# Kernel tuning notes

Hardware: AMD Instinct MI355X
Metric: run time of the kernel (lower is better)

## Reference

```python
import jax, jax.numpy as jnp
import numpy as np

N = 25000
E = 400000
H = 4        # heads
C = 256      # per-head channels
D_IN = 1024
NEG_SLOPE = 0.2


def setup_inputs() -> dict:
    key = jax.random.key(0)
    k1, k2, k3, k4, k5, k6 = jax.random.split(key, 6)
    x = jax.random.normal(k1, (N, D_IN), dtype=jnp.float32)
    edge_index = jax.random.randint(k2, (2, E), 0, N, dtype=jnp.int64)
    # GATConv parameters
    scale = 1.0 / np.sqrt(D_IN)
    W = jax.random.normal(k3, (D_IN, H * C), dtype=jnp.float32) * scale
    att_src = jax.random.normal(k4, (H, C), dtype=jnp.float32) * 0.1
    att_dst = jax.random.normal(k5, (H, C), dtype=jnp.float32) * 0.1
    bias = jax.random.normal(k6, (H * C,), dtype=jnp.float32) * 0.01
    return {"x": x, "edge_index": edge_index, "W": W,
            "att_src": att_src, "att_dst": att_dst, "bias": bias}


def reference(x, edge_index, W, att_src, att_dst, bias):
    # Dense projection: [N, D_IN] @ [D_IN, H*C] -> [N, H, C]
    xp = (x @ W).reshape(N, H, C)

    # Per-node attention logits [N, H]
    a_src = jnp.einsum('nhc,hc->nh', xp, att_src)
    a_dst = jnp.einsum('nhc,hc->nh', xp, att_dst)

    # PyG default add_self_loops=True
    loops = jnp.arange(N, dtype=edge_index.dtype)
    src = jnp.concatenate([edge_index[0], loops])  # [E+N]
    dst = jnp.concatenate([edge_index[1], loops])  # [E+N]

    # Edge attention logits + LeakyReLU
    e = jax.nn.leaky_relu(a_src[src] + a_dst[dst], NEG_SLOPE)  # [E+N, H]

    # Segment softmax over destination nodes (every node has a self loop)
    m = jax.ops.segment_max(e, dst, num_segments=N)            # [N, H]
    ee = jnp.exp(e - m[dst])
    z = jax.ops.segment_sum(ee, dst, num_segments=N)           # [N, H]
    alpha = ee / z[dst]                                        # [E+N, H]

    # Scatter-weighted aggregation: out[i] = sum_j alpha_ij * xp[j]
    msgs = xp[src] * alpha[:, :, None]                         # [E+N, H, C]
    out = jax.ops.segment_sum(msgs, dst, num_segments=N)       # [N, H, C]

    out = out.reshape(N, H * C) + bias
    # dropout(0.5) is identity in eval mode; act = ReLU
    return jax.nn.relu(out)
```

## Files before the change

### kernel.cpp

```cpp
#include <hip/hip_runtime.h>
#include <hip/hip_bf16.h>
#include <stdint.h>

#define N_NODES 25000
#define M_PAD   25088
#define E_EDGES 400000
#define NE      (E_EDGES + N_NODES)
#define D_DIM   1024
#define NEG_SLOPE 0.2f
#define KMAX    64

using bf16x8  = __attribute__((ext_vector_type(8))) short;
using floatx4 = __attribute__((ext_vector_type(4))) float;
using ushort8 = __attribute__((ext_vector_type(8))) unsigned short;

__device__ __forceinline__ unsigned short f2bf(float f) {
    union { float f; unsigned u; } v{f};
    unsigned r = v.u + 0x7fffu + ((v.u >> 16) & 1u);
    return (unsigned short)(r >> 16);
}
__device__ __forceinline__ float bf2f(unsigned short s) {
    union { unsigned u; float f; } v{(unsigned)s << 16};
    return v.f;
}

__global__ __launch_bounds__(256) void k_prep(
        const float* __restrict__ x, const float* __restrict__ W,
        unsigned short* __restrict__ xb, unsigned short* __restrict__ Wt,
        int* __restrict__ cursor) {
    __shared__ float tile[32][33];
    const int b = blockIdx.x, t = threadIdx.x;
    if (b < 1024) {
        int bx = b & 31, by = b >> 5;
        int tx = t & 31, ty = t >> 5;
        #pragma unroll
        for (int i = 0; i < 32; i += 8)
            tile[ty + i][tx] = W[(size_t)(by * 32 + ty + i) * D_DIM + bx * 32 + tx];
        __syncthreads();
        #pragma unroll
        for (int i = 0; i < 32; i += 8)
            Wt[(size_t)(bx * 32 + ty + i) * D_DIM + by * 32 + tx] =
                f2bf(tile[tx][ty + i]);
        if (b < 98) {
            int idx = b * 256 + t;
            if (idx < N_NODES) cursor[idx] = 0;
        }
    } else {
        int i = (b - 1024) * 256 + t;
        int row = i >> 8;
        ushort4 o;
        if (row < N_NODES) {
            float4 v = ((const float4*)x)[i];
            o = make_ushort4(f2bf(v.x), f2bf(v.y), f2bf(v.z), f2bf(v.w));
        } else {
            o = make_ushort4(0, 0, 0, 0);
        }
        ((ushort4*)xb)[i] = o;
    }
}

__device__ __forceinline__ void stage_half16(
        const unsigned short* __restrict__ g,
        unsigned short* lds_half,
        int wave, int rl, int sl8) {
    #pragma unroll
    for (int j = 0; j < 2; ++j) {
        const int R = j * 64 + wave * 8;
        __builtin_amdgcn_global_load_lds(
            (const __attribute__((address_space(1))) void*)
                (g + (size_t)(R + rl) * 1024 + sl8),
            (__attribute__((address_space(3))) void*)(lds_half + R * 64),
            16, 0, 0);
    }
}

__global__ __launch_bounds__(512, 2) void k_gemm256(
        const unsigned short* __restrict__ A,
        const unsigned short* __restrict__ Bt,
        const float* __restrict__ att_src, const float* __restrict__ att_dst,
        unsigned short* __restrict__ C,
        float* __restrict__ a_src, float* __restrict__ a_dst) {
    __shared__ unsigned short lds[65536];

    const int tid  = threadIdx.x;
    const int wave = tid >> 6, lane = tid & 63;
    const int lrow = lane & 15, quad = lane >> 4;
    const int wm   = wave >> 2, wn = wave & 3;
    const int rl   = lane >> 3;
    const int sl8  = ((lane & 7) ^ rl) * 8;

    const int wg = (blockIdx.x & 7) * 49 + (blockIdx.x >> 3);
    const int m0 = (wg % 98) * 256;
    const int n0 = (wg / 98) * 256;

    const unsigned short* Am = A  + (size_t)m0 * 1024;
    const unsigned short* Bn = Bt + (size_t)n0 * 1024;

    const int colk0 = (quad * 8)      ^ ((lrow & 7) << 3);
    const int colk1 = (32 + quad * 8) ^ ((lrow & 7) << 3);

    floatx4 acc[8][4] = {};

    stage_half16(Bn,                          lds + 16384,               wave, rl, sl8);
    stage_half16(Bn + (size_t)128 * 1024,     lds + 16384 + 8192,        wave, rl, sl8);
    stage_half16(Am,                          lds,                       wave, rl, sl8);
    stage_half16(Am + (size_t)128 * 1024,     lds + 8192,                wave, rl, sl8);
    stage_half16(Bn + 64,                     lds + 49152,               wave, rl, sl8);
    stage_half16(Bn + (size_t)128 * 1024 + 64, lds + 49152 + 8192,       wave, rl, sl8);
    stage_half16(Am + 64,                     lds + 32768,               wave, rl, sl8);
    asm volatile("s_waitcnt vmcnt(6)" ::: "memory");
    __builtin_amdgcn_sched_barrier(0);
    __builtin_amdgcn_s_barrier();

    #pragma unroll 1
    for (int it = 0; it < 8; ++it) {
        const int t   = it * 2;
        const int kt1 = t * 64 + 64, kt2 = t * 64 + 128, kt3 = t * 64 + 192;
        const bool s1 = kt2 < 1024;
        const bool s2 = kt3 < 1024;
        #pragma unroll
        for (int hb = 0; hb < 2; ++hb) {
            const unsigned short* LAc = lds + hb * 32768;
            const unsigned short* LBc = LAc + 16384;
            bf16x8 bfr[4][2];
            #pragma unroll
            for (int q = 0; q < 4; ++q) {
                bf16x8 af[2][2];
                #pragma unroll
                for (int j = 0; j < 2; ++j) {
                    const int ar = (wm * 128 + (2 * q + j) * 16 + lrow) * 64;
                    af[j][0] = *(const bf16x8*)(LAc + ar + colk0);
                    af[j][1] = *(const bf16x8*)(LAc + ar + colk1);
                }
                if (q == 0) {
                    #pragma unroll
                    for (int ni = 0; ni < 4; ++ni) {
                        const int br = (wn * 64 + ni * 16 + lrow) * 64;
                        bfr[ni][0] = *(const bf16x8*)(LBc + br + colk0);
                        bfr[ni][1] = *(const bf16x8*)(LBc + br + colk1);
                    }
                }
                if (hb == 0) {
                    if (q == 0)
                        stage_half16(Am + (size_t)128 * 1024 + kt1,
                                     lds + 32768 + 8192, wave, rl, sl8);
                    if (q == 1 && s1)
                        stage_half16(Bn + kt2, lds + 16384, wave, rl, sl8);
                    if (q == 2 && s1)
                        stage_half16(Bn + (size_t)128 * 1024 + kt2,
                                     lds + 16384 + 8192, wave, rl, sl8);
                    if (q == 3 && s1)
                        stage_half16(Am + kt2, lds, wave, rl, sl8);
                } else {
                    if (q == 0 && s1)
                        stage_half16(Am + (size_t)128 * 1024 + kt2,
                                     lds + 8192, wave, rl, sl8);
                    if (q == 1 && s2)
                        stage_half16(Bn + kt3, lds + 49152, wave, rl, sl8);
                    if (q == 2 && s2)
                        stage_half16(Bn + (size_t)128 * 1024 + kt3,
                                     lds + 49152 + 8192, wave, rl, sl8);
                    if (q == 3 && s2)
                        stage_half16(Am + kt3, lds + 32768, wave, rl, sl8);
                }
                if (q == 3) {
                    const bool full = (hb == 0) ? s1 : s2;
                    if (full) asm volatile("s_waitcnt vmcnt(6)" ::: "memory");
                    else      asm volatile("s_waitcnt vmcnt(0)" ::: "memory");
                    __builtin_amdgcn_sched_barrier(0);
                }
                __builtin_amdgcn_s_barrier();
                asm volatile("s_waitcnt lgkmcnt(0)" ::: "memory");
                __builtin_amdgcn_sched_barrier(0);
                __builtin_amdgcn_s_setprio(1);
                #pragma unroll
                for (int j = 0; j < 2; ++j)
                    #pragma unroll
                    for (int ni = 0; ni < 4; ++ni) {
                        acc[2*q+j][ni] = __builtin_amdgcn_mfma_f32_16x16x32_bf16(
                            af[j][0], bfr[ni][0], acc[2*q+j][ni], 0, 0, 0);
                        acc[2*q+j][ni] = __builtin_amdgcn_mfma_f32_16x16x32_bf16(
                            af[j][1], bfr[ni][1], acc[2*q+j][ni], 0, 0, 0);
                    }
                __builtin_amdgcn_s_setprio(0);
                __builtin_amdgcn_s_barrier();
            }
        }
    }

    {
        const int h4 = n0 >> 8;
        float asv[4], adv[4];
        #pragma unroll
        for (int ni = 0; ni < 4; ++ni) {
            int gc = n0 + wn * 64 + ni * 16 + lrow;
            asv[ni] = att_src[gc];
            adv[ni] = att_dst[gc];
        }
        __syncthreads();
        float* red = (float*)lds;
        #pragma unroll
        for (int mi = 0; mi < 8; ++mi) {
            #pragma unroll
            for (int r = 0; r < 4; ++r) {
                float s = 0.f, d = 0.f;
                #pragma unroll
                for (int ni = 0; ni < 4; ++ni) {
                    s += acc[mi][ni][r] * asv[ni];
                    d += acc[mi][ni][r] * adv[ni];
                }
                #pragma unroll
                for (int off = 1; off < 16; off <<= 1) {
                    s += __shfl_xor(s, off);
                    d += __shfl_xor(d, off);
                }
                if (lrow == 0) {
                    int rowl = mi * 16 + quad * 4 + r;
                    red[((wn * 2 + wm) * 128 + rowl) * 2 + 0] = s;
                    red[((wn * 2 + wm) * 128 + rowl) * 2 + 1] = d;
                }
            }
        }
        __syncthreads();
        const int sd   = tid & 1;
        const int rowl = (tid >> 1) & 127;
        const int wmr  = tid >> 8;
        float v = red[((0 * 2 + wmr) * 128 + rowl) * 2 + sd]
                + red[((1 * 2 + wmr) * 128 + rowl) * 2 + sd]
                + red[((2 * 2 + wmr) * 128 + rowl) * 2 + sd]
                + red[((3 * 2 + wmr) * 128 + rowl) * 2 + sd];
        int gm = m0 + wmr * 128 + rowl;
        if (gm < N_NODES) {
            if (sd == 0) a_src[gm * 4 + h4] = v;
            else         a_dst[gm * 4 + h4] = v;
        }
    }

    #pragma unroll
    for (int mi = 0; mi < 8; ++mi)
        #pragma unroll
        for (int ni = 0; ni < 4; ++ni)
            #pragma unroll
            for (int r = 0; r < 4; ++r) {
                int gm = m0 + wm * 128 + mi * 16 + quad * 4 + r;
                int gn = n0 + wn * 64 + ni * 16 + lrow;
                C[(size_t)gm * 1024 + gn] = f2bf(acc[mi][ni][r]);
            }
}

__global__ __launch_bounds__(256) void k_edge_exp_scatter(
        const int* __restrict__ ei,
        const float* __restrict__ a_src, const float* __restrict__ a_dst,
        int* __restrict__ cursor,
        int* __restrict__ csr_src, float* __restrict__ csr_ee) {
    int e = blockIdx.x * 256 + threadIdx.x;
    if (e >= NE) return;
    int s, d;
    if (e < E_EDGES) { s = ei[e]; d = ei[E_EDGES + e]; }
    else             { s = d = e - E_EDGES; }
    float4 as = *(const float4*)(&a_src[s * 4]);
    float4 ad = *(const float4*)(&a_dst[d * 4]);
    float l0 = as.x + ad.x, l1 = as.y + ad.y, l2 = as.z + ad.z, l3 = as.w + ad.w;
    l0 = l0 > 0.f ? l0 : NEG_SLOPE * l0;
    l1 = l1 > 0.f ? l1 : NEG_SLOPE * l1;
    l2 = l2 > 0.f ? l2 : NEG_SLOPE * l2;
    l3 = l3 > 0.f ? l3 : NEG_SLOPE * l3;
    int pos = atomicAdd(&cursor[d], 1);
    if (pos < KMAX) {
        int slot = d * KMAX + pos;
        csr_src[slot] = s;
        *(float4*)(&csr_ee[(size_t)slot * 4]) =
            make_float4(__expf(l0), __expf(l1), __expf(l2), __expf(l3));
    }
}

__device__ __forceinline__ void acc8(float* acc, float a, ushort8 v) {
    #pragma unroll
    for (int j = 0; j < 8; ++j) acc[j] += a * bf2f((unsigned short)v[j]);
}

__global__ __launch_bounds__(256) void k_node_aggregate(
        const int* __restrict__ csr_src, const float* __restrict__ csr_ee,
        const int* __restrict__ degc,
        const unsigned short* __restrict__ xp,
        const float* __restrict__ bias, float* __restrict__ out) {
    const int tid   = threadIdx.x;
    const int wave  = tid >> 6;
    const int lane  = tid & 63;
    const int n     = blockIdx.x * 2 + (wave >> 1);
    const int chalf = wave & 1;
    const int row   = n * KMAX;
    int deg = degc[n];
    deg = deg < KMAX ? deg : KMAX;

    float z0 = 0.f, z1 = 0.f, z2 = 0.f, z3 = 0.f;
    if (lane < deg) {
        float4 v = *(const float4*)(&csr_ee[(size_t)(row + lane) * 4]);
        z0 = v.x; z1 = v.y; z2 = v.z; z3 = v.w;
    }
    #pragma unroll
    for (int off = 32; off > 0; off >>= 1) {
        z0 += __shfl_down(z0, off);
        z1 += __shfl_down(z1, off);
        z2 += __shfl_down(z2, off);
        z3 += __shfl_down(z3, off);
    }
    z0 = __shfl(z0, 0); z1 = __shfl(z1, 0);
    z2 = __shfl(z2, 0); z3 = __shfl(z3, 0);

    const int c = chalf * 512 + lane * 8;
    const int h = c >> 8;
    const float rz = 1.0f / (chalf ? (lane >= 32 ? z3 : z2)
                                   : (lane >= 32 ? z1 : z0));

    float acc[8] = {};
    int i = 0;
    for (; i + 8 <= deg; i += 8) {
        int s[8];
        float a[8];
        #pragma unroll
        for (int u = 0; u < 8; ++u) s[u] = csr_src[row + i + u];
        #pragma unroll
        for (int u = 0; u < 8; ++u) a[u] = csr_ee[(size_t)(row + i + u) * 4 + h];
        ushort8 v[8];
        #pragma unroll
        for (int u = 0; u < 8; ++u)
            v[u] = *(const ushort8*)(&xp[(size_t)s[u] * D_DIM + c]);
        #pragma unroll
        for (int u = 0; u < 8; ++u) acc8(acc, a[u], v[u]);
    }
    for (; i + 4 <= deg; i += 4) {
        int s0 = csr_src[row + i + 0];
        int s1 = csr_src[row + i + 1];
        int s2 = csr_src[row + i + 2];
        int s3 = csr_src[row + i + 3];
        float a0 = csr_ee[(size_t)(row + i + 0) * 4 + h];
        float a1 = csr_ee[(size_t)(row + i + 1) * 4 + h];
        float a2 = csr_ee[(size_t)(row + i + 2) * 4 + h];
        float a3 = csr_ee[(size_t)(row + i + 3) * 4 + h];
        ushort8 v0 = *(const ushort8*)(&xp[(size_t)s0 * D_DIM + c]);
        ushort8 v1 = *(const ushort8*)(&xp[(size_t)s1 * D_DIM + c]);
        ushort8 v2 = *(const ushort8*)(&xp[(size_t)s2 * D_DIM + c]);
        ushort8 v3 = *(const ushort8*)(&xp[(size_t)s3 * D_DIM + c]);
        acc8(acc, a0, v0);
        acc8(acc, a1, v1);
        acc8(acc, a2, v2);
        acc8(acc, a3, v3);
    }
    for (; i < deg; ++i) {
        int s   = csr_src[row + i];
        float a = csr_ee[(size_t)(row + i) * 4 + h];
        ushort8 v = *(const ushort8*)(&xp[(size_t)s * D_DIM + c]);
        acc8(acc, a, v);
    }
    #pragma unroll
    for (int j = 0; j < 8; ++j) acc[j] *= rz;

    float4 b0 = *(const float4*)(&bias[c]);
    float4 b1 = *(const float4*)(&bias[c + 4]);
    float4 o0, o1;
    o0.x = fmaxf(acc[0] + b0.x, 0.f);
    o0.y = fmaxf(acc[1] + b0.y, 0.f);
    o0.z = fmaxf(acc[2] + b0.z, 0.f);
    o0.w = fmaxf(acc[3] + b0.w, 0.f);
    o1.x = fmaxf(acc[4] + b1.x, 0.f);
    o1.y = fmaxf(acc[5] + b1.y, 0.f);
    o1.z = fmaxf(acc[6] + b1.z, 0.f);
    o1.w = fmaxf(acc[7] + b1.w, 0.f);
    *(float4*)(&out[(size_t)n * D_DIM + c])     = o0;
    *(float4*)(&out[(size_t)n * D_DIM + c + 4]) = o1;
}

extern "C" void kernel_launch(void* const* d_in, const int* in_sizes, int n_in,
                              void* d_out, int out_size, void* d_ws, size_t ws_size,
                              hipStream_t stream) {
    const float* x       = (const float*)d_in[0];
    const int*   ei      = (const int*)d_in[1];
    const float* W       = (const float*)d_in[2];
    const float* att_src = (const float*)d_in[3];
    const float* att_dst = (const float*)d_in[4];
    const float* bias    = (const float*)d_in[5];
    float* out = (float*)d_out;

    char* ws = (char*)d_ws;
    size_t off = 0;
    auto alloc = [&](size_t bytes) -> void* {
        void* p = ws + off;
        off = (off + bytes + 255) & ~(size_t)255;
        return p;
    };
    unsigned short* xb   = (unsigned short*)alloc((size_t)M_PAD * D_DIM * 2);
    unsigned short* Wt   = (unsigned short*)alloc((size_t)D_DIM * D_DIM * 2);
    unsigned short* xpb  = (unsigned short*)alloc((size_t)M_PAD * D_DIM * 2);
    float* a_src    = (float*)alloc((size_t)N_NODES * 4 * 4);
    float* a_dst    = (float*)alloc((size_t)N_NODES * 4 * 4);
    int*   cursor   = (int*)alloc((size_t)N_NODES * 4);
    int*   csr_src  = (int*)alloc((size_t)N_NODES * KMAX * 4);
    float* csr_ee   = (float*)alloc((size_t)N_NODES * KMAX * 4 * 4);

    k_prep<<<1024 + M_PAD, 256, 0, stream>>>(x, W, xb, Wt, cursor);
    k_gemm256<<<dim3(M_PAD / 256 * (D_DIM / 256)), 512, 0, stream>>>(
        xb, Wt, att_src, att_dst, xpb, a_src, a_dst);
    k_edge_exp_scatter<<<(NE + 255) / 256, 256, 0, stream>>>(
        ei, a_src, a_dst, cursor, csr_src, csr_ee);
    k_node_aggregate<<<12500, 256, 0, stream>>>(
        csr_src, csr_ee, cursor, xpb, bias, out);
}
```

Before: 406.6 us.

## Accumulate softmax denominators with atomics and split aggregation into three launches

The softmax denominator per destination node and head is now accumulated with float atomics in the edge-scatter kernel into a zeroed buffer. This removes the per-wave shuffle reduction in the aggregation kernel, which now just loads the precomputed sum. The x-to-bf16 conversion in the prep kernel handles four chunks per block, so it launches a quarter as many blocks. The aggregation is split into three launches over node ranges with a bounds guard. In exchange the edge kernel issues four extra atomics per edge, float summation order becomes nondeterministic, and there are two more kernel launches.

```diff
diff --git a/kernel.cpp b/kernel.cpp
--- a/kernel.cpp
+++ b/kernel.cpp
@@ -27,7 +27,7 @@
 __global__ __launch_bounds__(256) void k_prep(
         const float* __restrict__ x, const float* __restrict__ W,
         unsigned short* __restrict__ xb, unsigned short* __restrict__ Wt,
-        int* __restrict__ cursor) {
+        int* __restrict__ cursor, float* __restrict__ z) {
     __shared__ float tile[32][33];
     const int b = blockIdx.x, t = threadIdx.x;
     if (b < 1024) {
@@ -43,19 +43,25 @@
                 f2bf(tile[tx][ty + i]);
         if (b < 98) {
             int idx = b * 256 + t;
-            if (idx < N_NODES) cursor[idx] = 0;
+            if (idx < N_NODES) {
+                cursor[idx] = 0;
+                *(float4*)(&z[idx * 4]) = make_float4(0.f, 0.f, 0.f, 0.f);
+            }
         }
     } else {
-        int i = (b - 1024) * 256 + t;
-        int row = i >> 8;
-        ushort4 o;
-        if (row < N_NODES) {
-            float4 v = ((const float4*)x)[i];
-            o = make_ushort4(f2bf(v.x), f2bf(v.y), f2bf(v.z), f2bf(v.w));
-        } else {
-            o = make_ushort4(0, 0, 0, 0);
-        }
-        ((ushort4*)xb)[i] = o;
+        #pragma unroll
+        for (int j = 0; j < 4; ++j) {
+            int i = (b - 1024) * 1024 + j * 256 + t;
+            int row = i >> 8;
+            ushort4 o;
+            if (row < N_NODES) {
+                float4 v = ((const float4*)x)[i];
+                o = make_ushort4(f2bf(v.x), f2bf(v.y), f2bf(v.z), f2bf(v.w));
+            } else {
+                o = make_ushort4(0, 0, 0, 0);
+            }
+            ((ushort4*)xb)[i] = o;
+        }
     }
 }
 
@@ -252,7 +258,8 @@
         const int* __restrict__ ei,
         const float* __restrict__ a_src, const float* __restrict__ a_dst,
         int* __restrict__ cursor,
-        int* __restrict__ csr_src, float* __restrict__ csr_ee) {
+        int* __restrict__ csr_src, float* __restrict__ csr_ee,
+        float* __restrict__ z) {
     int e = blockIdx.x * 256 + threadIdx.x;
     if (e >= NE) return;
     int s, d;
@@ -265,12 +272,16 @@
     l1 = l1 > 0.f ? l1 : NEG_SLOPE * l1;
     l2 = l2 > 0.f ? l2 : NEG_SLOPE * l2;
     l3 = l3 > 0.f ? l3 : NEG_SLOPE * l3;
+    float e0 = __expf(l0), e1 = __expf(l1), e2 = __expf(l2), e3 = __expf(l3);
     int pos = atomicAdd(&cursor[d], 1);
     if (pos < KMAX) {
         int slot = d * KMAX + pos;
         csr_src[slot] = s;
-        *(float4*)(&csr_ee[(size_t)slot * 4]) =
-            make_float4(__expf(l0), __expf(l1), __expf(l2), __expf(l3));
+        *(float4*)(&csr_ee[(size_t)slot * 4]) = make_float4(e0, e1, e2, e3);
+        atomicAdd(&z[d * 4 + 0], e0);
+        atomicAdd(&z[d * 4 + 1], e1);
+        atomicAdd(&z[d * 4 + 2], e2);
+        atomicAdd(&z[d * 4 + 3], e3);
     }
 }
 
@@ -281,37 +292,23 @@
 
 __global__ __launch_bounds__(256) void k_node_aggregate(
         const int* __restrict__ csr_src, const float* __restrict__ csr_ee,
-        const int* __restrict__ degc,
+        const int* __restrict__ degc, const float* __restrict__ z,
         const unsigned short* __restrict__ xp,
-        const float* __restrict__ bias, float* __restrict__ out) {
+        const float* __restrict__ bias, float* __restrict__ out,
+        int node_base) {
     const int tid   = threadIdx.x;
     const int wave  = tid >> 6;
     const int lane  = tid & 63;
-    const int n     = blockIdx.x * 2 + (wave >> 1);
+    const int n     = node_base + blockIdx.x * 2 + (wave >> 1);
     const int chalf = wave & 1;
+    if (n >= N_NODES) return;
     const int row   = n * KMAX;
     int deg = degc[n];
     deg = deg < KMAX ? deg : KMAX;
 
-    float z0 = 0.f, z1 = 0.f, z2 = 0.f, z3 = 0.f;
-    if (lane < deg) {
-        float4 v = *(const float4*)(&csr_ee[(size_t)(row + lane) * 4]);
-        z0 = v.x; z1 = v.y; z2 = v.z; z3 = v.w;
-    }
-    #pragma unroll
-    for (int off = 32; off > 0; off >>= 1) {
-        z0 += __shfl_down(z0, off);
-        z1 += __shfl_down(z1, off);
-        z2 += __shfl_down(z2, off);
-        z3 += __shfl_down(z3, off);
-    }
-    z0 = __shfl(z0, 0); z1 = __shfl(z1, 0);
-    z2 = __shfl(z2, 0); z3 = __shfl(z3, 0);
-
     const int c = chalf * 512 + lane * 8;
     const int h = c >> 8;
-    const float rz = 1.0f / (chalf ? (lane >= 32 ? z3 : z2)
-                                   : (lane >= 32 ? z1 : z0));
+    const float rz = 1.0f / z[n * 4 + h];
 
     float acc[8] = {};
     int i = 0;
@@ -395,14 +392,19 @@
     float* a_src    = (float*)alloc((size_t)N_NODES * 4 * 4);
     float* a_dst    = (float*)alloc((size_t)N_NODES * 4 * 4);
     int*   cursor   = (int*)alloc((size_t)N_NODES * 4);
+    float* zbuf     = (float*)alloc((size_t)N_NODES * 4 * 4);
     int*   csr_src  = (int*)alloc((size_t)N_NODES * KMAX * 4);
     float* csr_ee   = (float*)alloc((size_t)N_NODES * KMAX * 4 * 4);
 
-    k_prep<<<1024 + M_PAD, 256, 0, stream>>>(x, W, xb, Wt, cursor);
+    k_prep<<<1024 + M_PAD / 4, 256, 0, stream>>>(x, W, xb, Wt, cursor, zbuf);
     k_gemm256<<<dim3(M_PAD / 256 * (D_DIM / 256)), 512, 0, stream>>>(
         xb, Wt, att_src, att_dst, xpb, a_src, a_dst);
     k_edge_exp_scatter<<<(NE + 255) / 256, 256, 0, stream>>>(
-        ei, a_src, a_dst, cursor, csr_src, csr_ee);
-    k_node_aggregate<<<12500, 256, 0, stream>>>(
-        csr_src, csr_ee, cursor, xpb, bias, out);
-}
+        ei, a_src, a_dst, cursor, csr_src, csr_ee, zbuf);
+    k_node_aggregate<<<4167, 256, 0, stream>>>(
+        csr_src, csr_ee, cursor, zbuf, xpb, bias, out, 0);
+    k_node_aggregate<<<4167, 256, 0, stream>>>(
+        csr_src, csr_ee, cursor, zbuf, xpb, bias, out, 8334);
+    k_node_aggregate<<<4166, 256, 0, stream>>>(
+        csr_src, csr_ee, cursor, zbuf, xpb, bias, out, 16668);
+}
```

After: 500.7 us. +23.1%, slower.

## Fold edge bucketing into prep kernel and compute attention exps in aggregate

Applied to the files above, without the earlier changes.

Moves the CSR bucketing of edges by destination (atomic cursor plus src write) into the prep kernel, where it is independent of the GEMM, and drops the separate edge-exp kernel. The aggregate kernel now recomputes the LeakyReLU/exp logits per neighbour from a_src/a_dst and keeps them in LDS, which removes the csr_ee buffer write and read. The GEMM tile mapping is also remapped so that consecutive workgroups share an M tile. The cursor is now zeroed with a memset, which adds one more launch on the stream.

```diff
diff --git a/kernel.cpp b/kernel.cpp
--- a/kernel.cpp
+++ b/kernel.cpp
@@ -9,6 +9,7 @@
 #define D_DIM   1024
 #define NEG_SLOPE 0.2f
 #define KMAX    64
+#define NBLK_E  ((NE + 255) / 256)
 
 using bf16x8  = __attribute__((ext_vector_type(8))) short;
 using floatx4 = __attribute__((ext_vector_type(4))) float;
@@ -26,8 +27,9 @@
 
 __global__ __launch_bounds__(256) void k_prep(
         const float* __restrict__ x, const float* __restrict__ W,
+        const int* __restrict__ ei,
         unsigned short* __restrict__ xb, unsigned short* __restrict__ Wt,
-        int* __restrict__ cursor) {
+        int* __restrict__ cursor, int* __restrict__ csr_src) {
     __shared__ float tile[32][33];
     const int b = blockIdx.x, t = threadIdx.x;
     if (b < 1024) {
@@ -41,11 +43,7 @@
         for (int i = 0; i < 32; i += 8)
             Wt[(size_t)(bx * 32 + ty + i) * D_DIM + by * 32 + tx] =
                 f2bf(tile[tx][ty + i]);
-        if (b < 98) {
-            int idx = b * 256 + t;
-            if (idx < N_NODES) cursor[idx] = 0;
-        }
-    } else {
+    } else if (b < 1024 + M_PAD) {
         int i = (b - 1024) * 256 + t;
         int row = i >> 8;
         ushort4 o;
@@ -56,6 +54,15 @@
             o = make_ushort4(0, 0, 0, 0);
         }
         ((ushort4*)xb)[i] = o;
+    } else {
+        int e = (b - 1024 - M_PAD) * 256 + t;
+        if (e < NE) {
+            int s, d;
+            if (e < E_EDGES) { s = ei[e]; d = ei[E_EDGES + e]; }
+            else             { s = d = e - E_EDGES; }
+            int pos = atomicAdd(&cursor[d], 1);
+            if (pos < KMAX) csr_src[d * KMAX + pos] = s;
+        }
     }
 }
 
@@ -90,8 +97,8 @@
     const int sl8  = ((lane & 7) ^ rl) * 8;
 
     const int wg = (blockIdx.x & 7) * 49 + (blockIdx.x >> 3);
-    const int m0 = (wg % 98) * 256;
-    const int n0 = (wg / 98) * 256;
+    const int m0 = (wg >> 2) * 256;
+    const int n0 = (wg & 3) * 256;
 
     const unsigned short* Am = A  + (size_t)m0 * 1024;
     const unsigned short* Bn = Bt + (size_t)n0 * 1024;
@@ -248,42 +255,17 @@
             }
 }
 
-__global__ __launch_bounds__(256) void k_edge_exp_scatter(
-        const int* __restrict__ ei,
+__device__ __forceinline__ void acc8(float* acc, float a, ushort8 v) {
+    #pragma unroll
+    for (int j = 0; j < 8; ++j) acc[j] += a * bf2f((unsigned short)v[j]);
+}
+
+__global__ __launch_bounds__(256) void k_node_aggregate(
+        const int* __restrict__ csr_src, const int* __restrict__ degc,
         const float* __restrict__ a_src, const float* __restrict__ a_dst,
-        int* __restrict__ cursor,
-        int* __restrict__ csr_src, float* __restrict__ csr_ee) {
-    int e = blockIdx.x * 256 + threadIdx.x;
-    if (e >= NE) return;
-    int s, d;
-    if (e < E_EDGES) { s = ei[e]; d = ei[E_EDGES + e]; }
-    else             { s = d = e - E_EDGES; }
-    float4 as = *(const float4*)(&a_src[s * 4]);
-    float4 ad = *(const float4*)(&a_dst[d * 4]);
-    float l0 = as.x + ad.x, l1 = as.y + ad.y, l2 = as.z + ad.z, l3 = as.w + ad.w;
-    l0 = l0 > 0.f ? l0 : NEG_SLOPE * l0;
-    l1 = l1 > 0.f ? l1 : NEG_SLOPE * l1;
-    l2 = l2 > 0.f ? l2 : NEG_SLOPE * l2;
-    l3 = l3 > 0.f ? l3 : NEG_SLOPE * l3;
-    int pos = atomicAdd(&cursor[d], 1);
-    if (pos < KMAX) {
-        int slot = d * KMAX + pos;
-        csr_src[slot] = s;
-        *(float4*)(&csr_ee[(size_t)slot * 4]) =
-            make_float4(__expf(l0), __expf(l1), __expf(l2), __expf(l3));
-    }
-}
-
-__device__ __forceinline__ void acc8(float* acc, float a, ushort8 v) {
-    #pragma unroll
-    for (int j = 0; j < 8; ++j) acc[j] += a * bf2f((unsigned short)v[j]);
-}
-
-__global__ __launch_bounds__(256) void k_node_aggregate(
-        const int* __restrict__ csr_src, const float* __restrict__ csr_ee,
-        const int* __restrict__ degc,
         const unsigned short* __restrict__ xp,
         const float* __restrict__ bias, float* __restrict__ out) {
+    __shared__ float eesh[4][64][4];
     const int tid   = threadIdx.x;
     const int wave  = tid >> 6;
     const int lane  = tid & 63;
@@ -293,10 +275,20 @@
     int deg = degc[n];
     deg = deg < KMAX ? deg : KMAX;
 
+    const float4 ad = *(const float4*)(&a_dst[n * 4]);
+
     float z0 = 0.f, z1 = 0.f, z2 = 0.f, z3 = 0.f;
     if (lane < deg) {
-        float4 v = *(const float4*)(&csr_ee[(size_t)(row + lane) * 4]);
-        z0 = v.x; z1 = v.y; z2 = v.z; z3 = v.w;
+        int s = csr_src[row + lane];
+        float4 as = *(const float4*)(&a_src[s * 4]);
+        float l0 = as.x + ad.x, l1 = as.y + ad.y;
+        float l2 = as.z + ad.z, l3 = as.w + ad.w;
+        l0 = l0 > 0.f ? l0 : NEG_SLOPE * l0;
+        l1 = l1 > 0.f ? l1 : NEG_SLOPE * l1;
+        l2 = l2 > 0.f ? l2 : NEG_SLOPE * l2;
+        l3 = l3 > 0.f ? l3 : NEG_SLOPE * l3;
+        z0 = __expf(l0); z1 = __expf(l1); z2 = __expf(l2); z3 = __expf(l3);
+        *(float4*)(&eesh[wave][lane][0]) = make_float4(z0, z1, z2, z3);
     }
     #pragma unroll
     for (int off = 32; off > 0; off >>= 1) {
@@ -310,8 +302,8 @@
 
     const int c = chalf * 512 + lane * 8;
     const int h = c >> 8;
-    const float rz = 1.0f / (chalf ? (lane >= 32 ? z3 : z2)
-                                   : (lane >= 32 ? z1 : z0));
+    const float rz = 1.0f / (chalf ? (h == 3 ? z3 : z2)
+                                   : (h == 1 ? z1 : z0));
 
     float acc[8] = {};
     int i = 0;
@@ -321,7 +313,7 @@
         #pragma unroll
         for (int u = 0; u < 8; ++u) s[u] = csr_src[row + i + u];
         #pragma unroll
-        for (int u = 0; u < 8; ++u) a[u] = csr_ee[(size_t)(row + i + u) * 4 + h];
+        for (int u = 0; u < 8; ++u) a[u] = eesh[wave][i + u][h];
         ushort8 v[8];
         #pragma unroll
         for (int u = 0; u < 8; ++u)
@@ -334,10 +326,10 @@
         int s1 = csr_src[row + i + 1];
         int s2 = csr_src[row + i + 2];
         int s3 = csr_src[row + i + 3];
-        float a0 = csr_ee[(size_t)(row + i + 0) * 4 + h];
-        float a1 = csr_ee[(size_t)(row + i + 1) * 4 + h];
-        float a2 = csr_ee[(size_t)(row + i + 2) * 4 + h];
-        float a3 = csr_ee[(size_t)(row + i + 3) * 4 + h];
+        float a0 = eesh[wave][i + 0][h];
+        float a1 = eesh[wave][i + 1][h];
+        float a2 = eesh[wave][i + 2][h];
+        float a3 = eesh[wave][i + 3][h];
         ushort8 v0 = *(const ushort8*)(&xp[(size_t)s0 * D_DIM + c]);
         ushort8 v1 = *(const ushort8*)(&xp[(size_t)s1 * D_DIM + c]);
         ushort8 v2 = *(const ushort8*)(&xp[(size_t)s2 * D_DIM + c]);
@@ -349,7 +341,7 @@
     }
     for (; i < deg; ++i) {
         int s   = csr_src[row + i];
-        float a = csr_ee[(size_t)(row + i) * 4 + h];
+        float a = eesh[wave][i][h];
         ushort8 v = *(const ushort8*)(&xp[(size_t)s * D_DIM + c]);
         acc8(acc, a, v);
     }
@@ -396,13 +388,12 @@
     float* a_dst    = (float*)alloc((size_t)N_NODES * 4 * 4);
     int*   cursor   = (int*)alloc((size_t)N_NODES * 4);
     int*   csr_src  = (int*)alloc((size_t)N_NODES * KMAX * 4);
-    float* csr_ee   = (float*)alloc((size_t)N_NODES * KMAX * 4 * 4);
-
-    k_prep<<<1024 + M_PAD, 256, 0, stream>>>(x, W, xb, Wt, cursor);
+
+    hipMemsetAsync(cursor, 0, (size_t)N_NODES * 4, stream);
+    k_prep<<<1024 + M_PAD + NBLK_E, 256, 0, stream>>>(
+        x, W, ei, xb, Wt, cursor, csr_src);
     k_gemm256<<<dim3(M_PAD / 256 * (D_DIM / 256)), 512, 0, stream>>>(
         xb, Wt, att_src, att_dst, xpb, a_src, a_dst);
-    k_edge_exp_scatter<<<(NE + 255) / 256, 256, 0, stream>>>(
-        ei, a_src, a_dst, cursor, csr_src, csr_ee);
     k_node_aggregate<<<12500, 256, 0, stream>>>(
-        csr_src, csr_ee, cursor, xpb, bias, out);
-}
+        csr_src, cursor, a_src, a_dst, xpb, bias, out);
+}
```

Result: no change. 402.1 us (median of 2 runs) (-1.1%).
